# Kernel tuning notes

Hardware: AMD Instinct MI355X
Metric: run time of the kernel (lower is better)

## Reference

```python
import jax, jax.numpy as jnp
from jax import lax
import numpy as np

B, T, V, E, U = 1024, 80, 50000, 512, 512


def setup_inputs() -> dict:
    key = jax.random.key(0)
    ks = jax.random.split(key, 6)
    return {
        "tokens": jax.random.randint(ks[0], (B, T), 0, V, dtype=jnp.int32),
        "emb": jax.random.normal(ks[1], (V, E), jnp.float32) * 0.05,
        "kernel": jax.random.normal(ks[2], (E, U), jnp.float32) * (1.0 / np.sqrt(E)),
        "rec_kernel": jax.random.normal(ks[3], (U, U), jnp.float32) * (1.0 / np.sqrt(U)),
        "bias": jnp.zeros((U,), jnp.float32),
        "fc_w": jax.random.normal(ks[4], (U, 1), jnp.float32) * (1.0 / np.sqrt(U)),
        "fc_b": jnp.zeros((1,), jnp.float32),
    }


def reference(tokens, emb, kernel, rec_kernel, bias, fc_w, fc_b):
    # Embedding lookup: [B, T] -> [B, T, E]
    x = emb[tokens]
    # Precompute input projection for all timesteps (one big GEMM): [B, T, U]
    xk = jnp.einsum("bte,eu->btu", x, kernel) + bias
    h0 = jnp.zeros((tokens.shape[0], rec_kernel.shape[0]), dtype=emb.dtype)

    def step(h, xt):  # SimpleRNNCell (eval mode): h' = tanh(x@W + h@R + b)
        h_new = jnp.tanh(xt + h @ rec_kernel)
        return h_new, None

    h_final, _ = lax.scan(step, h0, jnp.swapaxes(xk, 0, 1))  # scan over T
    logits = h_final @ fc_w + fc_b  # [B, 1]
    return jax.nn.sigmoid(logits)
```

## Files before the change

### kernel.cpp

```cpp
#include <hip/hip_runtime.h>
#include <stdint.h>

constexpr int NB = 1024;
constexpr int NT = 80;
constexpr int NV = 50000;
constexpr int NE = 512;
constexpr int NU = 512;

typedef __attribute__((ext_vector_type(8))) __bf16 bf16x8;
typedef __attribute__((ext_vector_type(4))) float f32x4;
typedef __attribute__((ext_vector_type(4))) uint16_t u16x4;
typedef __attribute__((ext_vector_type(4))) float float4v;
typedef __attribute__((ext_vector_type(4))) uint32_t u32x4;

__device__ __forceinline__ uint16_t f2bf(float f) {
  uint32_t u = __builtin_bit_cast(uint32_t, f);
  u += 0x7FFFu + ((u >> 16) & 1u);
  return (uint16_t)(u >> 16);
}
__device__ __forceinline__ float bf2f(uint16_t h) {
  uint32_t u = ((uint32_t)h) << 16;
  return __builtin_bit_cast(float, u);
}
__device__ __forceinline__ float tanh_fast(float x) {
  float e = __expf(2.0f * x);
  return 1.0f - 2.0f / (e + 1.0f);
}

__device__ __forceinline__ void store16_cc(uint16_t* p, u32x4 v) {
  asm volatile("global_store_dwordx4 %0, %1, off sc0 sc1" :: "v"(p), "v"(v) : "memory");
}
__device__ __forceinline__ u32x4 load16_cc(const uint16_t* p) {
  u32x4 r;
  asm volatile("global_load_dwordx4 %0, %1, off sc0 sc1" : "=v"(r) : "v"(p) : "memory");
  return r;
}


__global__ __launch_bounds__(256) void emb_to_bf16(const float* __restrict__ in,
                                                   uint16_t* __restrict__ out) {
  int i = blockIdx.x * 256 + threadIdx.x;
  float4v v = ((const float4v*)in)[i];
  u16x4 o;
  o.x = f2bf(v.x); o.y = f2bf(v.y); o.z = f2bf(v.z); o.w = f2bf(v.w);
  ((u16x4*)out)[i] = o;
}

__global__ __launch_bounds__(256) void pack_w(const float* __restrict__ w,
                                              uint16_t* __restrict__ out) {
  int idx = blockIdx.x * 256 + threadIdx.x;
  int lane = idx & 63;
  int ks = (idx >> 6) & 15;
  int nt = idx >> 10;
  int n  = nt * 16 + (lane & 15);
  int k0 = ks * 32 + (lane >> 4) * 8;
  uint16_t v[8];
#pragma unroll
  for (int j = 0; j < 8; j++) v[j] = f2bf(w[(size_t)(k0 + j) * NU + n]);
  u16x4* o = (u16x4*)(out + (size_t)idx * 8);
  o[0] = (u16x4){v[0], v[1], v[2], v[3]};
  o[1] = (u16x4){v[4], v[5], v[6], v[7]};
}

__global__ __launch_bounds__(256, 2) void proj_gemm(const int* __restrict__ tokens,
                                                    const uint16_t* __restrict__ embb,
                                                    const uint16_t* __restrict__ kpack,
                                                    const float* __restrict__ bias,
                                                    uint16_t* __restrict__ xkp) {
  int wave = threadIdx.x >> 6;
  int lane = threadIdx.x & 63;
  int ln15 = lane & 15;
  int quad = lane >> 4;
  int m0 = blockIdx.x * 64;
  int t = m0 >> 10;
  int b0 = m0 & 1023;

  int tok[4];
#pragma unroll
  for (int mt = 0; mt < 4; mt++)
    tok[mt] = tokens[(size_t)(b0 + mt * 16 + ln15) * NT + t];

  float bv[8];
#pragma unroll
  for (int nt = 0; nt < 8; nt++) bv[nt] = bias[wave * 128 + nt * 16 + ln15];

  f32x4 acc[4][8];
#pragma unroll
  for (int mt = 0; mt < 4; mt++)
#pragma unroll
    for (int nt = 0; nt < 8; nt++) acc[mt][nt] = (f32x4){0.f, 0.f, 0.f, 0.f};

  bf16x8 aC[4], aN[4];
#pragma unroll
  for (int mt = 0; mt < 4; mt++) {
    aC[mt] = *(const bf16x8*)(embb + (size_t)tok[mt] * NE + 0 * 32 + quad * 8);
    aN[mt] = *(const bf16x8*)(embb + (size_t)tok[mt] * NE + 1 * 32 + quad * 8);
  }

#pragma unroll 1
  for (int ks = 0; ks < 16; ks++) {
    bf16x8 aF[4];
    int ksn = (ks + 2) & 15;
#pragma unroll
    for (int mt = 0; mt < 4; mt++)
      aF[mt] = *(const bf16x8*)(embb + (size_t)tok[mt] * NE + ksn * 32 + quad * 8);
#pragma unroll
    for (int nt = 0; nt < 8; nt++) {
      int ntg = wave * 8 + nt;
      bf16x8 bfr = *(const bf16x8*)(kpack + (((size_t)ntg * 16 + ks) * 64 + lane) * 8);
#pragma unroll
      for (int mt = 0; mt < 4; mt++)
        acc[mt][nt] = __builtin_amdgcn_mfma_f32_16x16x32_bf16(aC[mt], bfr, acc[mt][nt], 0, 0, 0);
    }
#pragma unroll
    for (int mt = 0; mt < 4; mt++) { aC[mt] = aN[mt]; aN[mt] = aF[mt]; }
  }

#pragma unroll
  for (int mt = 0; mt < 4; mt++) {
    int g = (b0 >> 4) + mt;
#pragma unroll
    for (int nt = 0; nt < 8; nt++) {
      int ntg = wave * 8 + nt;
      size_t tile = ((size_t)t * 64 + g) * 32 + ntg;
      u16x4 o;
      o.x = f2bf(acc[mt][nt][0] + bv[nt]);
      o.y = f2bf(acc[mt][nt][1] + bv[nt]);
      o.z = f2bf(acc[mt][nt][2] + bv[nt]);
      o.w = f2bf(acc[mt][nt][3] + bv[nt]);
      *(u16x4*)(xkp + tile * 256 + (size_t)lane * 4) = o;
    }
  }
}

__global__ __launch_bounds__(256, 1)
void rnn_rec(const uint16_t* __restrict__ xkp,
             const uint16_t* __restrict__ rpack,
             const float* __restrict__ fcw,
             const float* __restrict__ fcb,
             uint16_t* __restrict__ hx,
             int* __restrict__ flags,
             float* __restrict__ out) {
  __shared__ uint16_t hS[2 * 8192];

  const int bid = blockIdx.x;
  const int g = bid & 63, s = bid >> 6;
  const int wave = threadIdx.x >> 6, lane = threadIdx.x & 63;
  const int ln15 = lane & 15, quad = lane >> 4;
  const int ntg0 = s * 8 + wave * 2;
  const int aswz = quad ^ ((ln15 >> 1) & 3);

  bf16x8 bf0[16], bf1[16];
#pragma unroll
  for (int ks = 0; ks < 16; ks++) {
    bf0[ks] = *(const bf16x8*)(rpack + (((size_t)(ntg0 + 0) * 16 + ks) * 64 + lane) * 8);
    bf1[ks] = *(const bf16x8*)(rpack + (((size_t)(ntg0 + 1) * 16 + ks) * 64 + lane) * 8);
  }

  {
    u32x4 z = (u32x4){0u, 0u, 0u, 0u};
#pragma unroll
    for (int i = 0; i < 8; i++) ((u32x4*)hS)[i * 256 + threadIdx.x] = z;
  }
  __syncthreads();

  const int regionOwn = s * 4 + wave;
  int* flagOwn = flags + (g * 4 + s) * 16 + wave;

  u16x4 xc0 = *(const u16x4*)(xkp + (((size_t)0 * 64 + g) * 32 + ntg0 + 0) * 256 + (size_t)lane * 4);
  u16x4 xc1 = *(const u16x4*)(xkp + (((size_t)0 * 64 + g) * 32 + ntg0 + 1) * 256 + (size_t)lane * 4);

  for (int t = 0; t < NT; t++) {
    const int cur = t & 1;
    const uint16_t* hR = hS + cur * 8192;
    uint16_t* hW = hS + (cur ^ 1) * 8192;

    f32x4 acc0 = (f32x4){0.f, 0.f, 0.f, 0.f};
    f32x4 acc1 = (f32x4){0.f, 0.f, 0.f, 0.f};
#pragma unroll
    for (int ks = 0; ks < 16; ks++) {
      bf16x8 a = *(const bf16x8*)(hR + (size_t)ks * 512 + ln15 * 32 + aswz * 8);
      acc0 = __builtin_amdgcn_mfma_f32_16x16x32_bf16(a, bf0[ks], acc0, 0, 0, 0);
      acc1 = __builtin_amdgcn_mfma_f32_16x16x32_bf16(a, bf1[ks], acc1, 0, 0, 0);
    }

    uint16_t hv0[4], hv1[4];
#pragma unroll
    for (int r = 0; r < 4; r++) {
      hv0[r] = f2bf(tanh_fast(acc0[r] + bf2f(xc0[r])));
      hv1[r] = f2bf(tanh_fast(acc1[r] + bf2f(xc1[r])));
    }

#pragma unroll
    for (int i = 0; i < 2; i++) {
      const uint16_t* hv = (i == 0) ? hv0 : hv1;
      int col128 = (wave * 2 + i) * 16 + ln15;
      int qw = (col128 >> 3) & 3, j = col128 & 7;
#pragma unroll
      for (int r = 0; r < 4; r++) {
        int row = quad * 4 + r;
        hW[(size_t)regionOwn * 512 + row * 32 + (qw ^ ((row >> 1) & 3)) * 8 + j] = hv[r];
      }
    }
    asm volatile("s_waitcnt lgkmcnt(0)" ::: "memory");

    {
      u32x4 d = *(const u32x4*)(hW + (size_t)regionOwn * 512 + (size_t)lane * 8);
      uint16_t* dst = hx + ((size_t)((t + 1) & 1) * 256 + g * 4 + s) * 2048 +
                      (size_t)wave * 512 + (size_t)lane * 8;
      store16_cc(dst, d);
      asm volatile("s_waitcnt vmcnt(0)" ::: "memory");
      if (lane == 0)
        __hip_atomic_store(flagOwn, t + 1, __ATOMIC_RELAXED, __HIP_MEMORY_SCOPE_AGENT);
    }

    {
      int tn = (t + 1 < NT) ? (t + 1) : t;
      xc0 = *(const u16x4*)(xkp + (((size_t)tn * 64 + g) * 32 + ntg0 + 0) * 256 + (size_t)lane * 4);
      xc1 = *(const u16x4*)(xkp + (((size_t)tn * 64 + g) * 32 + ntg0 + 1) * 256 + (size_t)lane * 4);
    }

    if (wave > 0 && (t < NT - 1 || s == 0)) {
      int sp = (s + wave) & 3;
      const int* fp = flags + (g * 4 + sp) * 16;
      int spin = 0;
      for (;;) {
        u32x4 f = load16_cc((const uint16_t*)fp);
        asm volatile("s_waitcnt vmcnt(0)" ::: "memory");
        if ((int)f.x >= t + 1 && (int)f.y >= t + 1 &&
            (int)f.z >= t + 1 && (int)f.w >= t + 1) break;
        if (++spin >= (1 << 16)) break;
      }
      const uint16_t* src = hx + ((size_t)((t + 1) & 1) * 256 + g * 4 + sp) * 2048;
      u32x4 v0 = load16_cc(src + (size_t)(0 * 64 + lane) * 8);
      u32x4 v1 = load16_cc(src + (size_t)(1 * 64 + lane) * 8);
      u32x4 v2 = load16_cc(src + (size_t)(2 * 64 + lane) * 8);
      u32x4 v3 = load16_cc(src + (size_t)(3 * 64 + lane) * 8);
      asm volatile("s_waitcnt vmcnt(0)" ::: "memory");
      *(u32x4*)(hW + (size_t)sp * 2048 + (size_t)(0 * 64 + lane) * 8) = v0;
      *(u32x4*)(hW + (size_t)sp * 2048 + (size_t)(1 * 64 + lane) * 8) = v1;
      *(u32x4*)(hW + (size_t)sp * 2048 + (size_t)(2 * 64 + lane) * 8) = v2;
      *(u32x4*)(hW + (size_t)sp * 2048 + (size_t)(3 * 64 + lane) * 8) = v3;
    }
    __syncthreads();
  }

  if (s == 0) {
    const uint16_t* hB = hS + (NT & 1) * 8192;
#pragma unroll
    for (int rr = 0; rr < 4; rr++) {
      int row = wave * 4 + rr;
      int slot = (lane & 3) ^ ((row >> 1) & 3);
      const uint16_t* hr = hB + (size_t)(lane >> 2) * 512 + row * 32 + slot * 8;
      float p = 0.f;
#pragma unroll
      for (int j = 0; j < 8; j++) p += bf2f(hr[j]) * fcw[lane * 8 + j];
#pragma unroll
      for (int off = 32; off; off >>= 1) p += __shfl_down(p, off);
      if (lane == 0) {
        float logit = p + fcb[0];
        out[g * 16 + row] = 1.0f / (1.0f + __expf(-logit));
      }
    }
  }
}

extern "C" void kernel_launch(void* const* d_in, const int* in_sizes, int n_in,
                              void* d_out, int out_size, void* d_ws, size_t ws_size,
                              hipStream_t stream) {
  const int* tokens   = (const int*)d_in[0];
  const float* emb    = (const float*)d_in[1];
  const float* kernel_w = (const float*)d_in[2];
  const float* rec_w  = (const float*)d_in[3];
  const float* bias   = (const float*)d_in[4];
  const float* fcw    = (const float*)d_in[5];
  const float* fcb    = (const float*)d_in[6];
  float* out = (float*)d_out;

  uint16_t* embb  = (uint16_t*)d_ws;
  uint16_t* kpack = embb + (size_t)NV * NE;
  uint16_t* rpack = kpack + (size_t)NE * NU;
  uint16_t* xkp   = rpack + (size_t)NU * NU;
  uint16_t* hx    = xkp + (size_t)NT * NB * NU;
  int* flags      = (int*)(hx + (size_t)2 * 256 * 2048);

  hipLaunchKernelGGL(emb_to_bf16, dim3(25000), dim3(256), 0, stream, emb, embb);
  hipLaunchKernelGGL(pack_w, dim3(128), dim3(256), 0, stream, kernel_w, kpack);
  hipLaunchKernelGGL(pack_w, dim3(128), dim3(256), 0, stream, rec_w, rpack);
  hipLaunchKernelGGL(proj_gemm, dim3(1280), dim3(256), 0, stream, tokens, embb, kpack, bias, xkp);
  hipLaunchKernelGGL(rnn_rec, dim3(256), dim3(256), 0, stream, xkp, rpack, fcw, fcb, hx, flags, out);
}
```

Measured before the change: 477.6 us.

## Split recurrent step across two 512-thread blocks per batch group instead of four

The recurrent kernel now runs 128 blocks of 8 waves, each owning half of the hidden units for a 16-row batch group, instead of 256 blocks of 4 waves each owning a quarter. Each wave now waits on a single partner flag and copies one 16-byte slice of the partner's hidden state, replacing the four-flag spin and four-vector copy. The aim is to cut the cross-block exchange and flag-polling cost on the serial per-timestep critical path. The next-step projection load is also issued before the spin wait. In exchange, per-CU register pressure rises and only 128 CUs are used.

```diff
diff --git a/kernel.cpp b/kernel.cpp
--- a/kernel.cpp
+++ b/kernel.cpp
@@ -133,7 +133,7 @@
   }
 }
 
-__global__ __launch_bounds__(256, 1)
+__global__ __launch_bounds__(512, 1)
 void rnn_rec(const uint16_t* __restrict__ xkp,
              const uint16_t* __restrict__ rpack,
              const float* __restrict__ fcw,
@@ -144,44 +144,53 @@
   __shared__ uint16_t hS[2 * 8192];
 
   const int bid = blockIdx.x;
-  const int g = bid & 63, s = bid >> 6;
+  const int g = bid >> 1, s = bid & 1;
   const int wave = threadIdx.x >> 6, lane = threadIdx.x & 63;
   const int ln15 = lane & 15, quad = lane >> 4;
-  const int ntg0 = s * 8 + wave * 2;
+  const int ntg0 = s * 16 + wave * 2;
   const int aswz = quad ^ ((ln15 >> 1) & 3);
 
-  bf16x8 bf0[16], bf1[16];
-#pragma unroll
-  for (int ks = 0; ks < 16; ks++) {
-    bf0[ks] = *(const bf16x8*)(rpack + (((size_t)(ntg0 + 0) * 16 + ks) * 64 + lane) * 8);
-    bf1[ks] = *(const bf16x8*)(rpack + (((size_t)(ntg0 + 1) * 16 + ks) * 64 + lane) * 8);
-  }
+  bf16x8 bP[16][2];
+#pragma unroll
+  for (int ks = 0; ks < 16; ks++)
+#pragma unroll
+    for (int n = 0; n < 2; n++)
+      bP[ks][n] = *(const bf16x8*)(rpack + (((size_t)(ntg0 + n) * 16 + ks) * 64 + lane) * 8);
+#pragma unroll
+  for (int ks = 0; ks < 16; ks++)
+    asm volatile("" : "+v"(bP[ks][0]), "+v"(bP[ks][1]));
 
   {
     u32x4 z = (u32x4){0u, 0u, 0u, 0u};
-#pragma unroll
-    for (int i = 0; i < 8; i++) ((u32x4*)hS)[i * 256 + threadIdx.x] = z;
-  }
+    ((u32x4*)hS)[threadIdx.x] = z;
+    ((u32x4*)hS)[512 + threadIdx.x] = z;
+  }
+
+  const int regionOwn = s * 8 + wave;
+  const int regionPar = (1 - s) * 8 + wave;
+  const int chunkOwn = g * 2 + s;
+  const int chunkPar = g * 2 + (1 - s);
+  int* flagOwn = flags + (chunkOwn * 8 + wave) * 4;
+  const int* flagPar = flags + (chunkPar * 8 + wave) * 4;
+
+  const uint16_t* xp = xkp + ((size_t)g * 32 + ntg0) * 256 + (size_t)lane * 4;
+  u16x4 xc0 = *(const u16x4*)(xp);
+  u16x4 xc1 = *(const u16x4*)(xp + 256);
+
   __syncthreads();
 
-  const int regionOwn = s * 4 + wave;
-  int* flagOwn = flags + (g * 4 + s) * 16 + wave;
-
-  u16x4 xc0 = *(const u16x4*)(xkp + (((size_t)0 * 64 + g) * 32 + ntg0 + 0) * 256 + (size_t)lane * 4);
-  u16x4 xc1 = *(const u16x4*)(xkp + (((size_t)0 * 64 + g) * 32 + ntg0 + 1) * 256 + (size_t)lane * 4);
-
-  for (int t = 0; t < NT; t++) {
-    const int cur = t & 1;
-    const uint16_t* hR = hS + cur * 8192;
-    uint16_t* hW = hS + (cur ^ 1) * 8192;
+#pragma unroll 1
+  for (int t = 0; t < NT; ++t) {
+    const uint16_t* hR = hS + (t & 1) * 8192;
+    uint16_t* hW = hS + ((t & 1) ^ 1) * 8192;
 
     f32x4 acc0 = (f32x4){0.f, 0.f, 0.f, 0.f};
     f32x4 acc1 = (f32x4){0.f, 0.f, 0.f, 0.f};
 #pragma unroll
     for (int ks = 0; ks < 16; ks++) {
       bf16x8 a = *(const bf16x8*)(hR + (size_t)ks * 512 + ln15 * 32 + aswz * 8);
-      acc0 = __builtin_amdgcn_mfma_f32_16x16x32_bf16(a, bf0[ks], acc0, 0, 0, 0);
-      acc1 = __builtin_amdgcn_mfma_f32_16x16x32_bf16(a, bf1[ks], acc1, 0, 0, 0);
+      acc0 = __builtin_amdgcn_mfma_f32_16x16x32_bf16(a, bP[ks][0], acc0, 0, 0, 0);
+      acc1 = __builtin_amdgcn_mfma_f32_16x16x32_bf16(a, bP[ks][1], acc1, 0, 0, 0);
     }
 
     uint16_t hv0[4], hv1[4];
@@ -192,21 +201,21 @@
     }
 
 #pragma unroll
-    for (int i = 0; i < 2; i++) {
-      const uint16_t* hv = (i == 0) ? hv0 : hv1;
-      int col128 = (wave * 2 + i) * 16 + ln15;
-      int qw = (col128 >> 3) & 3, j = col128 & 7;
+    for (int n = 0; n < 2; n++) {
+      const uint16_t* hv = (n == 0) ? hv0 : hv1;
+      int qw = n * 2 + (ln15 >> 3);
+      int j = ln15 & 7;
 #pragma unroll
       for (int r = 0; r < 4; r++) {
         int row = quad * 4 + r;
-        hW[(size_t)regionOwn * 512 + row * 32 + (qw ^ ((row >> 1) & 3)) * 8 + j] = hv[r];
+        hW[(size_t)regionOwn * 512 + row * 32 + ((qw ^ ((row >> 1) & 3)) << 3) + j] = hv[r];
       }
     }
     asm volatile("s_waitcnt lgkmcnt(0)" ::: "memory");
 
     {
       u32x4 d = *(const u32x4*)(hW + (size_t)regionOwn * 512 + (size_t)lane * 8);
-      uint16_t* dst = hx + ((size_t)((t + 1) & 1) * 256 + g * 4 + s) * 2048 +
+      uint16_t* dst = hx + ((size_t)((t + 1) & 1) * 128 + chunkOwn) * 4096 +
                       (size_t)wave * 512 + (size_t)lane * 8;
       store16_cc(dst, d);
       asm volatile("s_waitcnt vmcnt(0)" ::: "memory");
@@ -214,42 +223,32 @@
         __hip_atomic_store(flagOwn, t + 1, __ATOMIC_RELAXED, __HIP_MEMORY_SCOPE_AGENT);
     }
 
+    const uint16_t* xq = (t + 1 < NT) ? xp + (size_t)64 * 32 * 256 : xp;
+    u16x4 xn0 = *(const u16x4*)(xq);
+    u16x4 xn1 = *(const u16x4*)(xq + 256);
+    xp = xq;
+
     {
-      int tn = (t + 1 < NT) ? (t + 1) : t;
-      xc0 = *(const u16x4*)(xkp + (((size_t)tn * 64 + g) * 32 + ntg0 + 0) * 256 + (size_t)lane * 4);
-      xc1 = *(const u16x4*)(xkp + (((size_t)tn * 64 + g) * 32 + ntg0 + 1) * 256 + (size_t)lane * 4);
-    }
-
-    if (wave > 0 && (t < NT - 1 || s == 0)) {
-      int sp = (s + wave) & 3;
-      const int* fp = flags + (g * 4 + sp) * 16;
       int spin = 0;
-      for (;;) {
-        u32x4 f = load16_cc((const uint16_t*)fp);
-        asm volatile("s_waitcnt vmcnt(0)" ::: "memory");
-        if ((int)f.x >= t + 1 && (int)f.y >= t + 1 &&
-            (int)f.z >= t + 1 && (int)f.w >= t + 1) break;
-        if (++spin >= (1 << 16)) break;
-      }
-      const uint16_t* src = hx + ((size_t)((t + 1) & 1) * 256 + g * 4 + sp) * 2048;
-      u32x4 v0 = load16_cc(src + (size_t)(0 * 64 + lane) * 8);
-      u32x4 v1 = load16_cc(src + (size_t)(1 * 64 + lane) * 8);
-      u32x4 v2 = load16_cc(src + (size_t)(2 * 64 + lane) * 8);
-      u32x4 v3 = load16_cc(src + (size_t)(3 * 64 + lane) * 8);
+      while (__hip_atomic_load(flagPar, __ATOMIC_RELAXED, __HIP_MEMORY_SCOPE_AGENT) < t + 1 &&
+             spin < (1 << 18))
+        spin++;
+      const uint16_t* src = hx + ((size_t)((t + 1) & 1) * 128 + chunkPar) * 4096 +
+                            (size_t)wave * 512 + (size_t)lane * 8;
+      u32x4 v = load16_cc(src);
       asm volatile("s_waitcnt vmcnt(0)" ::: "memory");
-      *(u32x4*)(hW + (size_t)sp * 2048 + (size_t)(0 * 64 + lane) * 8) = v0;
-      *(u32x4*)(hW + (size_t)sp * 2048 + (size_t)(1 * 64 + lane) * 8) = v1;
-      *(u32x4*)(hW + (size_t)sp * 2048 + (size_t)(2 * 64 + lane) * 8) = v2;
-      *(u32x4*)(hW + (size_t)sp * 2048 + (size_t)(3 * 64 + lane) * 8) = v3;
-    }
+      *(u32x4*)(hW + (size_t)regionPar * 512 + (size_t)lane * 8) = v;
+    }
+
+    xc0 = xn0; xc1 = xn1;
     __syncthreads();
   }
 
   if (s == 0) {
     const uint16_t* hB = hS + (NT & 1) * 8192;
 #pragma unroll
-    for (int rr = 0; rr < 4; rr++) {
-      int row = wave * 4 + rr;
+    for (int rr = 0; rr < 2; rr++) {
+      int row = wave * 2 + rr;
       int slot = (lane & 3) ^ ((row >> 1) & 3);
       const uint16_t* hr = hB + (size_t)(lane >> 2) * 512 + row * 32 + slot * 8;
       float p = 0.f;
@@ -282,11 +281,11 @@
   uint16_t* rpack = kpack + (size_t)NE * NU;
   uint16_t* xkp   = rpack + (size_t)NU * NU;
   uint16_t* hx    = xkp + (size_t)NT * NB * NU;
-  int* flags      = (int*)(hx + (size_t)2 * 256 * 2048);
+  int* flags      = (int*)(hx + (size_t)2 * 128 * 4096);
 
   hipLaunchKernelGGL(emb_to_bf16, dim3(25000), dim3(256), 0, stream, emb, embb);
   hipLaunchKernelGGL(pack_w, dim3(128), dim3(256), 0, stream, kernel_w, kpack);
   hipLaunchKernelGGL(pack_w, dim3(128), dim3(256), 0, stream, rec_w, rpack);
   hipLaunchKernelGGL(proj_gemm, dim3(1280), dim3(256), 0, stream, tokens, embb, kpack, bias, xkp);
-  hipLaunchKernelGGL(rnn_rec, dim3(256), dim3(256), 0, stream, xkp, rpack, fcw, fcb, hx, flags, out);
-}
+  hipLaunchKernelGGL(rnn_rec, dim3(128), dim3(512), 0, stream, xkp, rpack, fcw, fcb, hx, flags, out);
+}
```

After: 474.2 us. Within noise of the previous version (-0.7%).
